# Kernel tuning notes

Measured on AMD Instinct MI355X. Metric: run time of the kernel, lower is better.

The kernel has to match this reference:

```python
import math
import jax, jax.numpy as jnp
import numpy as np

B, S, D = 8, 512, 1024        # batch, seq (dec and enc), model dim
HID, NH = 1024, 16            # attention hidden, heads
C = HID // NH                 # per-head channels (self-attn 'attends' over this dim!)
EPS = 1e-5


def setup_inputs() -> dict:
    key = jax.random.key(0)
    ks = jax.random.split(key, 26)
    w = lambda k, sh: (jax.random.normal(k, sh, jnp.float32) * 0.02)
    inp = {
        "x": jax.random.normal(ks[0], (B, S, D), jnp.float32),
        "h": jax.random.normal(ks[1], (B, S, D), jnp.float32),
        # self-attn (AttentionModule) params, stored [in, out]
        "Wq": w(ks[2], (D, HID)), "bq": jnp.zeros((HID,), jnp.float32),
        "Wk": w(ks[3], (D, HID)), "bk": jnp.zeros((HID,), jnp.float32),
        "Wv": w(ks[4], (D, HID)), "bv": jnp.zeros((HID,), jnp.float32),
        "Wo": w(ks[5], (HID, D)), "bo": jnp.zeros((D,), jnp.float32),
        # cross-attn params
        "Wcq": w(ks[6], (D, HID)), "bcq": jnp.zeros((HID,), jnp.float32),
        "Wck": w(ks[7], (D, HID)), "bck": jnp.zeros((HID,), jnp.float32),
        "Wcv": w(ks[8], (D, HID)), "bcv": jnp.zeros((HID,), jnp.float32),
        "Wco": w(ks[9], (HID, D)), "bco": jnp.zeros((D,), jnp.float32),
        "gamma": jnp.ones((D,), jnp.float32), "beta": jnp.zeros((D,), jnp.float32),
        # FFN (two Linears, NO nonlinearity, per original code)
        "W1": w(ks[10], (D, HID)), "b1": jnp.zeros((HID,), jnp.float32),
        "W2": w(ks[11], (HID, D)), "b2": jnp.zeros((D,), jnp.float32),
    }
    return inp


def _layernorm(x, gamma, beta):
    mu = jnp.mean(x, axis=-1, keepdims=True)
    var = jnp.mean(jnp.square(x - mu), axis=-1, keepdims=True)
    return (x - mu) * jax.lax.rsqrt(var + EPS) * gamma + beta


def _self_attn(x, Wq, bq, Wk, bk, Wv, bv, Wo, bo):
    # FAITHFUL to original: reshape [B,S,NH,C]; einsum '...hq,...hk->...hqk' with
    # batch dims [B,S] -> attention over the C channel dim per token, causal mask over channels.
    Q = (x @ Wq + bq).reshape(B, S, NH, C) / math.sqrt(C)
    K = (x @ Wk + bk).reshape(B, S, NH, C)
    V = (x @ Wv + bv).reshape(B, S, NH, C)
    aff = jnp.einsum('bshq,bshk->bshqk', Q, K)            # [B,S,NH,C,C]
    mask = jnp.triu(jnp.full((C, C), -jnp.inf, jnp.float32), k=1)  # -inf above diag, 0 else
    aff = aff + mask
    w = jax.nn.softmax(aff, axis=-1)
    av = jnp.einsum('bshqk,bshk->bshq', w, V)             # [B,S,NH,C]
    return av.reshape(B, S, HID) @ Wo + bo


def _cross_attn(xd, he, Wcq, bcq, Wck, bck, Wcv, bcv, Wco, bco):
    # standard multi-head cross attention, but scaled by sqrt(d_full) per original
    Q = (xd @ Wcq + bcq).reshape(B, S, NH, C).transpose(0, 2, 1, 3)  # [B,NH,Sq,C]
    K = (he @ Wck + bck).reshape(B, S, NH, C).transpose(0, 2, 1, 3)
    V = (he @ Wcv + bcv).reshape(B, S, NH, C).transpose(0, 2, 1, 3)
    scores = jnp.einsum('bhqd,bhkd->bhqk', Q, K) / math.sqrt(HID)
    p = jax.nn.softmax(scores, axis=-1)
    o = jnp.einsum('bhqk,bhkd->bhqd', p, V)               # [B,NH,Sq,C]
    o = o.transpose(0, 2, 1, 3).reshape(B, S, HID)
    return o @ Wco + bco


def reference(x, h, Wq, bq, Wk, bk, Wv, bv, Wo, bo,
              Wcq, bcq, Wck, bck, Wcv, bcv, Wco, bco,
              gamma, beta, W1, b1, W2, b2):
    out = _self_attn(x, Wq, bq, Wk, bk, Wv, bv, Wo, bo) + x
    out = _layernorm(out, gamma, beta)
    out = _cross_attn(out, h, Wcq, bcq, Wck, bck, Wcv, bcv, Wco, bco) + out
    out = _layernorm(out, gamma, beta)
    out = ((out @ W1 + b1) @ W2 + b2) + out
    out = _layernorm(out, gamma, beta)
    return out
```

## Files before the change

kernel.cpp:

```cpp
#include <hip/hip_runtime.h>

typedef __bf16 bf16_t;
typedef bf16_t bf16x8 __attribute__((ext_vector_type(8)));
typedef bf16_t bf16x4 __attribute__((ext_vector_type(4)));
typedef float f32x4 __attribute__((ext_vector_type(4)));

__device__ __forceinline__ void async_copy16(const void* g, void* l) {
  __builtin_amdgcn_global_load_lds(
      (const __attribute__((address_space(1))) unsigned int*)(unsigned long long)g,
      (__attribute__((address_space(3))) unsigned int*)(unsigned int)(unsigned long long)l,
      16, 0, 0);
}

__device__ __forceinline__ float fast_exp2(float x) {
#if __has_builtin(__builtin_amdgcn_exp2f)
  return __builtin_amdgcn_exp2f(x);
#else
  return exp2f(x);
#endif
}

__device__ __forceinline__ unsigned pack_bf16(float x, float y) {
  bf16_t lo = (bf16_t)x, hi = (bf16_t)y;
  unsigned short ul, uh;
  __builtin_memcpy(&ul, &lo, 2);
  __builtin_memcpy(&uh, &hi, 2);
  return (unsigned)ul | ((unsigned)uh << 16);
}

__global__ __launch_bounds__(256) void cast3_bf16_kernel(
    const float* __restrict__ a, const float* __restrict__ b,
    const float* __restrict__ w1, bf16_t* __restrict__ dst1,
    bf16_t* __restrict__ dstw) {
  int i = (blockIdx.x * 256 + threadIdx.x) * 8;
  const float* s;
  bf16_t* d;
  if (i < 4194304) { s = a + i; d = dst1 + i; }
  else if (i < 8388608) { s = b + i - 4194304; d = dst1 + i; }
  else { s = w1 + i - 8388608; d = dstw + (i - 8388608); }
  float4 u = *(const float4*)s;
  float4 v = *(const float4*)(s + 4);
  bf16x8 o;
  o[0]=(bf16_t)u.x; o[1]=(bf16_t)u.y; o[2]=(bf16_t)u.z; o[3]=(bf16_t)u.w;
  o[4]=(bf16_t)v.x; o[5]=(bf16_t)v.y; o[6]=(bf16_t)v.z; o[7]=(bf16_t)v.w;
  *(bf16x8*)d = o;
}

struct SrcPtrs { const float* p[10]; };
__global__ __launch_bounds__(256) void transpose_cast_all(
    SrcPtrs srcs, bf16_t* __restrict__ dstbase) {
  __shared__ float tile[32][33];
  int z = blockIdx.z;
  const float* src = srcs.p[z];
  bf16_t* dst = dstbase + (size_t)z * 1048576;
  float scale = (z == 0) ? 0.125f : ((z == 4) ? 0.03125f : 1.f);
  int bx = blockIdx.x * 32;
  int by = blockIdx.y * 32;
  int tx = threadIdx.x, ty = threadIdx.y;
#pragma unroll
  for (int i = 0; i < 32; i += 8)
    tile[ty + i][tx] = src[(size_t)(by + ty + i) * 1024 + bx + tx];
  __syncthreads();
#pragma unroll
  for (int i = 0; i < 32; i += 8)
    dst[(size_t)(bx + ty + i) * 1024 + by + tx] = (bf16_t)(tile[tx][ty + i] * scale);
}

__global__ __launch_bounds__(256) void prep_bias_kernel(
    const float* __restrict__ bq, const float* __restrict__ bk,
    const float* __restrict__ bv, const float* __restrict__ bck,
    const float* __restrict__ bcv, const float* __restrict__ bcq,
    const bf16_t* __restrict__ wt9, const float* __restrict__ b1,
    const float* __restrict__ b2, float* __restrict__ cb,
    float* __restrict__ cb2) {
  int bid = blockIdx.x;
  if (bid < 28) {
    int i = bid * 256 + threadIdx.x;
    if (i < 1024) cb[i] = bq[i] * 0.125f;
    else if (i < 2048) cb[i] = bk[i - 1024];
    else if (i < 3072) cb[i] = bv[i - 2048];
    else if (i < 4096) cb[i] = bck[i - 3072];
    else if (i < 5120) cb[i] = bcv[i - 4096];
    else if (i < 6144) cb[i] = bcq[i - 5120] * 0.03125f;
    else cb[i] = 0.f;
  } else {
    int n = (bid - 28) * 256 + threadIdx.x;
    const bf16_t* row = wt9 + (size_t)n * 1024;
    float acc = 0.f;
#pragma unroll 4
    for (int h = 0; h < 1024; h += 8) {
      bf16x8 v = *(const bf16x8*)(row + h);
      float4 ba = *(const float4*)(b1 + h);
      float4 bb = *(const float4*)(b1 + h + 4);
      acc += ba.x*(float)v[0] + ba.y*(float)v[1] + ba.z*(float)v[2] + ba.w*(float)v[3]
           + bb.x*(float)v[4] + bb.y*(float)v[5] + bb.z*(float)v[6] + bb.w*(float)v[7];
    }
    cb2[n] = acc + b2[n];
  }
}

template <int BN, int MI, bool HAS_RES, bool TRANS_OUT>
__device__ __forceinline__ void gemm_core(
    const bf16_t* __restrict__ A, const bf16_t* __restrict__ Bt,
    const float* __restrict__ bias, const bf16_t* __restrict__ res,
    bf16_t* __restrict__ C, int ldC, int bm, int bn,
    bf16_t* As, bf16_t* Bs) {
  constexpr int NI = 4;
  int tid = threadIdx.x;
  int w = tid >> 6, lane = tid & 63;
  int fm = lane & 15, fq = lane >> 4;
  int wm = (BN == 128) ? (w >> 1) * 64 : w * 32;
  int wn = (BN == 128) ? (w & 1) * 64 : 0;
  f32x4 acc[MI][NI] = {};
  for (int kt = 0; kt < 1024; kt += 64) {
#pragma unroll
    for (int i = 0; i < 4; i++) {
      int c = i * 256 + tid;
      int row = c >> 3, skg = (c & 7) ^ (row & 7);
      async_copy16(A + (size_t)(bm + row) * 1024 + kt + skg * 8, &As[c * 8]);
    }
#pragma unroll
    for (int i = 0; i < BN / 32; i++) {
      int c = i * 256 + tid;
      int row = c >> 3, skg = (c & 7) ^ (row & 7);
      async_copy16(Bt + (size_t)(bn + row) * 1024 + kt + skg * 8, &Bs[c * 8]);
    }
    __syncthreads();
#pragma unroll
    for (int ks = 0; ks < 2; ks++) {
      bf16x8 af[MI], bfr[NI];
      int kg = ks * 4 + fq;
#pragma unroll
      for (int mi = 0; mi < MI; mi++) {
        int row = wm + mi * 16 + fm;
        af[mi] = *(const bf16x8*)&As[row * 64 + ((kg ^ (row & 7)) * 8)];
      }
#pragma unroll
      for (int ni = 0; ni < NI; ni++) {
        int row = wn + ni * 16 + fm;
        bfr[ni] = *(const bf16x8*)&Bs[row * 64 + ((kg ^ (row & 7)) * 8)];
      }
#pragma unroll
      for (int mi = 0; mi < MI; mi++)
#pragma unroll
        for (int ni = 0; ni < NI; ni++)
          acc[mi][ni] = __builtin_amdgcn_mfma_f32_16x16x32_bf16(
              af[mi], bfr[ni], acc[mi][ni], 0, 0, 0);
    }
    __syncthreads();
  }
#pragma unroll
  for (int mi = 0; mi < MI; mi++) {
#pragma unroll
    for (int ni = 0; ni < NI; ni++) {
      int col = bn + wn + ni * 16 + fm;
      float bv = bias[col];
      if (TRANS_OUT) {
        int rowb = bm + wm + mi * 16 + fq * 4;
        bf16x4 w4;
#pragma unroll
        for (int r = 0; r < 4; r++) w4[r] = (bf16_t)(acc[mi][ni][r] + bv);
        *(bf16x4*)&C[(size_t)col * ldC + rowb] = w4;
      } else {
#pragma unroll
        for (int r = 0; r < 4; r++) {
          int row = bm + wm + mi * 16 + fq * 4 + r;
          float v = acc[mi][ni][r] + bv;
          if (HAS_RES) v += (float)res[(size_t)row * ldC + col];
          C[(size_t)row * ldC + col] = (bf16_t)v;
        }
      }
    }
  }
}

template <int GX, int GY, int BN>
__device__ __forceinline__ void xcd_map(int lin, int& bm, int& bn) {
  constexpr int HX = GX / 2, QY = GY / 4;
  int xcd = lin & 7, idx = lin >> 3;
  int ly = idx / HX, lx = idx - ly * HX;
  bm = ((xcd >> 1) * QY + ly) * 128;
  bn = ((xcd & 1) * HX + lx) * BN;
}

template <bool HAS_RES, bool TRANS_OUT>
__global__ __launch_bounds__(256) void gemm_bf16(
    const bf16_t* __restrict__ A, const bf16_t* __restrict__ Bt,
    const float* __restrict__ bias, const bf16_t* __restrict__ res,
    bf16_t* __restrict__ C, int ldC) {
  __shared__ bf16_t As[128 * 64];
  __shared__ bf16_t Bs[64 * 64];
  int bm, bn;
  xcd_map<16, 32, 64>(blockIdx.x + 16 * blockIdx.y, bm, bn);
  gemm_core<64, 2, HAS_RES, TRANS_OUT>(A, Bt, bias, res, C, ldC, bm, bn, As, Bs);
}

__global__ __launch_bounds__(256) void gemm_qkv_p(
    const bf16_t* __restrict__ xb, const bf16_t* __restrict__ wt0,
    const bf16_t* __restrict__ wt9, const bf16_t* __restrict__ w1bf,
    const float* __restrict__ cb, bf16_t* __restrict__ qkv,
    bf16_t* __restrict__ pt) {
  __shared__ bf16_t smem[2 * 128 * 64];
  int lin = blockIdx.x + 24 * blockIdx.y;
  if (blockIdx.z == 0) {
    int bm, bn;
    xcd_map<24, 32, 128>(lin, bm, bn);
    gemm_core<128, 4, false, false>(xb, wt0, cb, nullptr, qkv, 3072,
                                    bm, bn, smem, smem + 128 * 64);
  } else {
    if (lin >= 128) return;
    gemm_core<64, 2, false, false>(wt9, w1bf, cb + 6144, nullptr, pt, 1024,
                                   (lin >> 4) * 128, (lin & 15) * 64,
                                   smem, smem + 128 * 64);
  }
}

__global__ __launch_bounds__(256) void gemm_cqkv(
    const bf16_t* __restrict__ t1n, const bf16_t* __restrict__ hb,
    const bf16_t* __restrict__ wt4, const float* __restrict__ cb,
    bf16_t* __restrict__ cq, bf16_t* __restrict__ kbuf,
    bf16_t* __restrict__ vt) {
  __shared__ bf16_t As[128 * 64];
  __shared__ bf16_t Bs[64 * 64];
  int lin = blockIdx.x + 48 * blockIdx.y;
  int xcd = lin & 7, idx = lin >> 3;
  int ly = idx / 24, lx = idx - ly * 24;
  int bm = ((xcd >> 1) * 8 + ly) * 128;
  int gx = (xcd & 1) * 24 + lx;
  int region = gx >> 4;
  int bn = (gx & 15) * 64;
  const bf16_t* Bt = wt4 + (size_t)region * 1048576;
  if (region == 2) {
    gemm_core<64, 2, false, true>(hb, Bt, cb + 4096, nullptr, vt, 4096,
                                  bm, bn, As, Bs);
  } else if (region == 1) {
    gemm_core<64, 2, false, false>(hb, Bt, cb + 3072, nullptr, kbuf, 1024,
                                   bm, bn, As, Bs);
  } else {
    gemm_core<64, 2, false, false>(t1n, Bt, cb + 5120, nullptr, cq, 1024,
                                   bm, bn, As, Bs);
  }
}

__global__ __launch_bounds__(256) void self_attn_kernel(
    const bf16_t* __restrict__ QKV, bf16_t* __restrict__ O) {
  __shared__ float2 kv[4][64];
  int tid = threadIdx.x;
  int wu = tid >> 6, lane = tid & 63;
  int unit = blockIdx.x * 4 + wu;
  int m = unit >> 4, h = unit & 15;
  size_t iq = (size_t)m * 3072 + h * 64 + lane;
  float q = (float)QKV[iq] * 1.44269504089f;
  float kk = (float)QKV[iq + 1024];
  float vv = (float)QKV[iq + 2048];
  kv[wu][lane] = make_float2(kk, vv);
  __syncthreads();
  const float2* kvp = kv[wu];
  float l0 = 0.f, l1 = 0.f, o0 = 0.f, o1 = 0.f;
#pragma unroll
  for (int j = 0; j < 64; j += 2) {
    float2 a = kvp[j];
    float2 b = kvp[j + 1];
    float e0 = fast_exp2(q * a.x);
    float e1 = fast_exp2(q * b.x);
    e0 = (j <= lane) ? e0 : 0.f;
    e1 = (j + 1 <= lane) ? e1 : 0.f;
    l0 += e0; o0 = fmaf(e0, a.y, o0);
    l1 += e1; o1 = fmaf(e1, b.y, o1);
  }
  float l = l0 + l1, o = o0 + o1;
  O[(size_t)m * 1024 + h * 64 + lane] = (bf16_t)(o / l);
}

__global__ __launch_bounds__(256) void cross_attn_mfma(
    const bf16_t* __restrict__ Q, const bf16_t* __restrict__ Kb,
    const bf16_t* __restrict__ Vt, bf16_t* __restrict__ O) {
  __shared__ bf16_t Ks[64 * 64];
  __shared__ bf16_t Vs[64 * 64];
  int tid = threadIdx.x;
  int w = tid >> 6, lane = tid & 63;
  int fm = lane & 15, fq = lane >> 4;
  int bh = blockIdx.x;
  int b = bh >> 4, h = bh & 15;
  int q0 = blockIdx.y * 64 + w * 16;
  const bf16_t* Qp = Q + (size_t)(b * 512 + q0 + fm) * 1024 + h * 64 + fq * 8;
  bf16x8 qf0 = *(const bf16x8*)Qp;
  bf16x8 qf1 = *(const bf16x8*)(Qp + 32);
  f32x4 o[4] = {};
  float mx = -1e30f, l = 0.f;
  for (int k0 = 0; k0 < 512; k0 += 64) {
    __syncthreads();
#pragma unroll
    for (int i = 0; i < 2; i++) {
      int c = i * 256 + tid;
      int row = c >> 3, kg = (c & 7) ^ (row & 7);
      async_copy16(Kb + (size_t)(b * 512 + k0 + row) * 1024 + h * 64 + kg * 8,
                   &Ks[c * 8]);
      async_copy16(Vt + (size_t)(h * 64 + row) * 4096 + b * 512 + k0 + kg * 8,
                   &Vs[c * 8]);
    }
    __syncthreads();
    f32x4 s[4] = {};
#pragma unroll
    for (int mt = 0; mt < 4; mt++) {
      int row = mt * 16 + fm;
#pragma unroll
      for (int f = 0; f < 2; f++) {
        int kg = f * 4 + fq;
        bf16x8 kf = *(const bf16x8*)&Ks[row * 64 + ((kg ^ (row & 7)) * 8)];
        s[mt] = __builtin_amdgcn_mfma_f32_16x16x32_bf16(
            kf, (f ? qf1 : qf0), s[mt], 0, 0, 0);
      }
    }
    float smax = -1e30f;
#pragma unroll
    for (int mt = 0; mt < 4; mt++)
#pragma unroll
      for (int r = 0; r < 4; r++) smax = fmaxf(smax, s[mt][r]);
    smax = fmaxf(smax, __shfl_xor(smax, 16, 64));
    smax = fmaxf(smax, __shfl_xor(smax, 32, 64));
    float nm = fmaxf(mx, smax);
    float corr = __expf(mx - nm);
    float ladd = 0.f;
    unsigned pk0[4], pk1[4];
#pragma unroll
    for (int mt = 0; mt < 4; mt++) {
      float p0 = __expf(s[mt][0] - nm);
      float p1 = __expf(s[mt][1] - nm);
      float p2 = __expf(s[mt][2] - nm);
      float p3 = __expf(s[mt][3] - nm);
      ladd += (p0 + p1) + (p2 + p3);
      pk0[mt] = pack_bf16(p0, p1);
      pk1[mt] = pack_bf16(p2, p3);
    }
    ladd += __shfl_xor(ladd, 16, 64);
    ladd += __shfl_xor(ladd, 32, 64);
    l = l * corr + ladd;
#pragma unroll
    for (int ct = 0; ct < 4; ct++)
#pragma unroll
      for (int r = 0; r < 4; r++) o[ct][r] *= corr;
    union U { unsigned u[4]; bf16x8 v; } pf[2];
    int sl0 = ((fq & 1) * 2) * 16 + fm;
    int sl1 = sl0 + 16;
    bool hi = fq >= 2;
#pragma unroll
    for (int f = 0; f < 2; f++) {
      unsigned a0 = (unsigned)__shfl((int)pk0[f * 2],     sl0, 64);
      unsigned b0 = (unsigned)__shfl((int)pk0[f * 2 + 1], sl0, 64);
      unsigned a1 = (unsigned)__shfl((int)pk1[f * 2],     sl0, 64);
      unsigned b1 = (unsigned)__shfl((int)pk1[f * 2 + 1], sl0, 64);
      unsigned a2 = (unsigned)__shfl((int)pk0[f * 2],     sl1, 64);
      unsigned b2 = (unsigned)__shfl((int)pk0[f * 2 + 1], sl1, 64);
      unsigned a3 = (unsigned)__shfl((int)pk1[f * 2],     sl1, 64);
      unsigned b3 = (unsigned)__shfl((int)pk1[f * 2 + 1], sl1, 64);
      pf[f].u[0] = hi ? b0 : a0;
      pf[f].u[1] = hi ? b1 : a1;
      pf[f].u[2] = hi ? b2 : a2;
      pf[f].u[3] = hi ? b3 : a3;
    }
#pragma unroll
    for (int ct = 0; ct < 4; ct++) {
      int row = ct * 16 + fm;
#pragma unroll
      for (int f = 0; f < 2; f++) {
        int kg = f * 4 + fq;
        bf16x8 vf = *(const bf16x8*)&Vs[row * 64 + ((kg ^ (row & 7)) * 8)];
        o[ct] = __builtin_amdgcn_mfma_f32_16x16x32_bf16(vf, pf[f].v, o[ct], 0, 0, 0);
      }
    }
    mx = nm;
  }
  float inv = 1.f / l;
  bf16_t* Op = O + (size_t)(b * 512 + q0 + fm) * 1024 + h * 64 + fq * 4;
#pragma unroll
  for (int ct = 0; ct < 4; ct++) {
    bf16x4 w4;
    w4[0] = (bf16_t)(o[ct][0] * inv);
    w4[1] = (bf16_t)(o[ct][1] * inv);
    w4[2] = (bf16_t)(o[ct][2] * inv);
    w4[3] = (bf16_t)(o[ct][3] * inv);
    *(bf16x4*)(Op + ct * 16) = w4;
  }
}

template <typename OutT>
__global__ __launch_bounds__(256) void ln_kernel(
    const bf16_t* __restrict__ X, const float* __restrict__ gamma,
    const float* __restrict__ beta, OutT* __restrict__ Y) {
  __shared__ float red[8];
  int row = blockIdx.x;
  int tid = threadIdx.x;
  bf16x4 x4 = *(const bf16x4*)(X + (size_t)row * 1024 + tid * 4);
  float4 v = {(float)x4[0], (float)x4[1], (float)x4[2], (float)x4[3]};
  float s = (v.x + v.y) + (v.z + v.w);
  float ss = fmaf(v.x, v.x, fmaf(v.y, v.y, fmaf(v.z, v.z, v.w * v.w)));
#pragma unroll
  for (int off = 32; off > 0; off >>= 1) {
    s  += __shfl_down(s, off, 64);
    ss += __shfl_down(ss, off, 64);
  }
  if ((tid & 63) == 0) { red[tid >> 6] = s; red[4 + (tid >> 6)] = ss; }
  __syncthreads();
  float S  = (red[0] + red[1]) + (red[2] + red[3]);
  float SS = (red[4] + red[5]) + (red[6] + red[7]);
  float mu = S * (1.f / 1024.f);
  float var = SS * (1.f / 1024.f) - mu * mu;
  float inv = rsqrtf(var + 1e-5f);
  float4 g = *(const float4*)(gamma + tid * 4);
  float4 b = *(const float4*)(beta + tid * 4);
  float r0 = (v.x - mu) * inv * g.x + b.x;
  float r1 = (v.y - mu) * inv * g.y + b.y;
  float r2 = (v.z - mu) * inv * g.z + b.z;
  float r3 = (v.w - mu) * inv * g.w + b.w;
  OutT* yp = Y + (size_t)row * 1024 + tid * 4;
  yp[0] = (OutT)r0; yp[1] = (OutT)r1; yp[2] = (OutT)r2; yp[3] = (OutT)r3;
}

extern "C" void kernel_launch(void* const* d_in, const int* in_sizes, int n_in,
                              void* d_out, int out_size, void* d_ws, size_t ws_size,
                              hipStream_t stream) {
  (void)in_sizes; (void)n_in; (void)out_size; (void)ws_size;
  const float* x  = (const float*)d_in[0];
  const float* hh = (const float*)d_in[1];
  SrcPtrs sp;
  sp.p[0] = (const float*)d_in[2];  sp.p[1] = (const float*)d_in[4];
  sp.p[2] = (const float*)d_in[6];  sp.p[3] = (const float*)d_in[8];
  sp.p[4] = (const float*)d_in[10]; sp.p[5] = (const float*)d_in[12];
  sp.p[6] = (const float*)d_in[14]; sp.p[7] = (const float*)d_in[16];
  sp.p[8] = (const float*)d_in[20]; sp.p[9] = (const float*)d_in[22];
  const float* W1f = (const float*)d_in[20];
  const float* bq  = (const float*)d_in[3];
  const float* bk  = (const float*)d_in[5];
  const float* bv  = (const float*)d_in[7];
  const float* bo  = (const float*)d_in[9];
  const float* bck = (const float*)d_in[13];
  const float* bcv = (const float*)d_in[15];
  const float* bcq = (const float*)d_in[11];
  const float* bco = (const float*)d_in[17];
  const float* gamma = (const float*)d_in[18];
  const float* beta  = (const float*)d_in[19];
  const float* b1  = (const float*)d_in[21];
  const float* b2  = (const float*)d_in[23];
  float* out = (float*)d_out;
  char* ws = (char*)d_ws;
  const size_t MB = 1048576;

  bf16_t* wt[10];
  for (int i = 0; i < 10; i++) wt[i] = (bf16_t*)(ws + (size_t)i * 2 * MB);
  float* cb      = (float*)(ws + 20 * MB);
  float* cb2     = (float*)(ws + 20 * MB + 32768);
  bf16_t* xb     = (bf16_t*)(ws + 21 * MB);
  bf16_t* hb     = (bf16_t*)(ws + 29 * MB);
  bf16_t* qkv    = (bf16_t*)(ws + 37 * MB);
  bf16_t* kbuf   = (bf16_t*)(ws + 37 * MB);
  bf16_t* vtbuf  = (bf16_t*)(ws + 45 * MB);
  bf16_t* cqbuf  = (bf16_t*)(ws + 61 * MB);
  bf16_t* attn   = (bf16_t*)(ws + 69 * MB);
  bf16_t* g4     = (bf16_t*)(ws + 77 * MB);
  bf16_t* ptbuf  = (bf16_t*)(ws + 85 * MB);
  bf16_t* w1bf   = (bf16_t*)(ws + 87 * MB);
  bf16_t* t1n    = xb;
  bf16_t* t2n    = hb;
  bf16_t* f2out  = g4;

  cast3_bf16_kernel<<<4608, 256, 0, stream>>>(x, hh, W1f, xb, w1bf);
  transpose_cast_all<<<dim3(32, 32, 10), dim3(32, 8), 0, stream>>>(sp, (bf16_t*)ws);
  prep_bias_kernel<<<32, 256, 0, stream>>>(bq, bk, bv, bck, bcv, bcq,
                                           wt[9], b1, b2, cb, cb2);

  gemm_qkv_p<<<dim3(24, 32, 2), 256, 0, stream>>>(xb, wt[0], wt[9], w1bf, cb, qkv, ptbuf);
  self_attn_kernel<<<16384, 256, 0, stream>>>(qkv, attn);
  gemm_bf16<true, false><<<dim3(16, 32), 256, 0, stream>>>(attn, wt[3], bo, xb, g4, 1024);
  ln_kernel<bf16_t><<<4096, 256, 0, stream>>>(g4, gamma, beta, t1n);
  gemm_cqkv<<<dim3(48, 32), 256, 0, stream>>>(t1n, hb, wt[4], cb, cqbuf, kbuf, vtbuf);
  cross_attn_mfma<<<dim3(128, 8), 256, 0, stream>>>(cqbuf, kbuf, vtbuf, attn);
  gemm_bf16<true, false><<<dim3(16, 32), 256, 0, stream>>>(attn, wt[7], bco, t1n, g4, 1024);
  ln_kernel<bf16_t><<<4096, 256, 0, stream>>>(g4, gamma, beta, t2n);
  gemm_bf16<true, false><<<dim3(16, 32), 256, 0, stream>>>(t2n, ptbuf, cb2, t2n, f2out, 1024);
  ln_kernel<float><<<4096, 256, 0, stream>>>(f2out, gamma, beta, out);
}
```

Baseline: 391.2 us.

## Double-buffer LDS in output GEMMs and merge prep kernel launches

Adds a double-buffered LDS path to the shared GEMM core so the next K tile's async loads overlap the MFMA work on the current tile, with one barrier per step, and uses it for the three 1024x1024 projection GEMMs. The cast and transpose prep kernels are merged into one launch. The QKV launch is reshaped into a flat grid that no longer spawns blocks that exit immediately. Doubling LDS use may reduce occupancy.

```diff
diff --git a/kernel.cpp b/kernel.cpp
--- a/kernel.cpp
+++ b/kernel.cpp
@@ -28,42 +28,45 @@
   return (unsigned)ul | ((unsigned)uh << 16);
 }
 
-__global__ __launch_bounds__(256) void cast3_bf16_kernel(
+struct SrcPtrs { const float* p[10]; };
+__global__ __launch_bounds__(256) void prep_main(
+    SrcPtrs srcs, bf16_t* __restrict__ dstbase,
     const float* __restrict__ a, const float* __restrict__ b,
     const float* __restrict__ w1, bf16_t* __restrict__ dst1,
     bf16_t* __restrict__ dstw) {
-  int i = (blockIdx.x * 256 + threadIdx.x) * 8;
-  const float* s;
-  bf16_t* d;
-  if (i < 4194304) { s = a + i; d = dst1 + i; }
-  else if (i < 8388608) { s = b + i - 4194304; d = dst1 + i; }
-  else { s = w1 + i - 8388608; d = dstw + (i - 8388608); }
-  float4 u = *(const float4*)s;
-  float4 v = *(const float4*)(s + 4);
-  bf16x8 o;
-  o[0]=(bf16_t)u.x; o[1]=(bf16_t)u.y; o[2]=(bf16_t)u.z; o[3]=(bf16_t)u.w;
-  o[4]=(bf16_t)v.x; o[5]=(bf16_t)v.y; o[6]=(bf16_t)v.z; o[7]=(bf16_t)v.w;
-  *(bf16x8*)d = o;
-}
-
-struct SrcPtrs { const float* p[10]; };
-__global__ __launch_bounds__(256) void transpose_cast_all(
-    SrcPtrs srcs, bf16_t* __restrict__ dstbase) {
   __shared__ float tile[32][33];
-  int z = blockIdx.z;
-  const float* src = srcs.p[z];
-  bf16_t* dst = dstbase + (size_t)z * 1048576;
-  float scale = (z == 0) ? 0.125f : ((z == 4) ? 0.03125f : 1.f);
-  int bx = blockIdx.x * 32;
-  int by = blockIdx.y * 32;
-  int tx = threadIdx.x, ty = threadIdx.y;
-#pragma unroll
-  for (int i = 0; i < 32; i += 8)
-    tile[ty + i][tx] = src[(size_t)(by + ty + i) * 1024 + bx + tx];
-  __syncthreads();
-#pragma unroll
-  for (int i = 0; i < 32; i += 8)
-    dst[(size_t)(bx + ty + i) * 1024 + by + tx] = (bf16_t)(tile[tx][ty + i] * scale);
+  int bid = blockIdx.x;
+  int tid = threadIdx.x;
+  if (bid < 10240) {
+    int z = bid >> 10;
+    int rem = bid & 1023;
+    const float* src = srcs.p[z];
+    bf16_t* dst = dstbase + (size_t)z * 1048576;
+    float scale = (z == 0) ? 0.125f : ((z == 4) ? 0.03125f : 1.f);
+    int bx = (rem & 31) * 32;
+    int by = (rem >> 5) * 32;
+    int tx = tid & 31, ty = tid >> 5;
+#pragma unroll
+    for (int i = 0; i < 32; i += 8)
+      tile[ty + i][tx] = src[(size_t)(by + ty + i) * 1024 + bx + tx];
+    __syncthreads();
+#pragma unroll
+    for (int i = 0; i < 32; i += 8)
+      dst[(size_t)(bx + ty + i) * 1024 + by + tx] = (bf16_t)(tile[tx][ty + i] * scale);
+  } else {
+    int i = ((bid - 10240) * 256 + tid) * 8;
+    const float* s;
+    bf16_t* d;
+    if (i < 4194304) { s = a + i; d = dst1 + i; }
+    else if (i < 8388608) { s = b + i - 4194304; d = dst1 + i; }
+    else { s = w1 + i - 8388608; d = dstw + (i - 8388608); }
+    float4 u = *(const float4*)s;
+    float4 v = *(const float4*)(s + 4);
+    bf16x8 o;
+    o[0]=(bf16_t)u.x; o[1]=(bf16_t)u.y; o[2]=(bf16_t)u.z; o[3]=(bf16_t)u.w;
+    o[4]=(bf16_t)v.x; o[5]=(bf16_t)v.y; o[6]=(bf16_t)v.z; o[7]=(bf16_t)v.w;
+    *(bf16x8*)d = o;
+  }
 }
 
 __global__ __launch_bounds__(256) void prep_bias_kernel(
@@ -99,33 +102,40 @@
   }
 }
 
-template <int BN, int MI, bool HAS_RES, bool TRANS_OUT>
+template <int BN, int MI, bool HAS_RES, bool TRANS_OUT, bool DBUF>
 __device__ __forceinline__ void gemm_core(
     const bf16_t* __restrict__ A, const bf16_t* __restrict__ Bt,
     const float* __restrict__ bias, const bf16_t* __restrict__ res,
     bf16_t* __restrict__ C, int ldC, int bm, int bn,
     bf16_t* As, bf16_t* Bs) {
   constexpr int NI = 4;
+  constexpr int ASZ = 128 * 64, BSZ = BN * 64;
   int tid = threadIdx.x;
   int w = tid >> 6, lane = tid & 63;
   int fm = lane & 15, fq = lane >> 4;
   int wm = (BN == 128) ? (w >> 1) * 64 : w * 32;
   int wn = (BN == 128) ? (w & 1) * 64 : 0;
   f32x4 acc[MI][NI] = {};
-  for (int kt = 0; kt < 1024; kt += 64) {
+
+  auto stage = [&](int kt, int half) {
+    bf16_t* Ad = DBUF ? As + half * ASZ : As;
+    bf16_t* Bd = DBUF ? Bs + half * BSZ : Bs;
 #pragma unroll
     for (int i = 0; i < 4; i++) {
       int c = i * 256 + tid;
       int row = c >> 3, skg = (c & 7) ^ (row & 7);
-      async_copy16(A + (size_t)(bm + row) * 1024 + kt + skg * 8, &As[c * 8]);
+      async_copy16(A + (size_t)(bm + row) * 1024 + kt + skg * 8, &Ad[c * 8]);
     }
 #pragma unroll
     for (int i = 0; i < BN / 32; i++) {
       int c = i * 256 + tid;
       int row = c >> 3, skg = (c & 7) ^ (row & 7);
-      async_copy16(Bt + (size_t)(bn + row) * 1024 + kt + skg * 8, &Bs[c * 8]);
-    }
-    __syncthreads();
+      async_copy16(Bt + (size_t)(bn + row) * 1024 + kt + skg * 8, &Bd[c * 8]);
+    }
+  };
+  auto compute = [&](int half) {
+    const bf16_t* Ac = DBUF ? As + half * ASZ : As;
+    const bf16_t* Bc = DBUF ? Bs + half * BSZ : Bs;
 #pragma unroll
     for (int ks = 0; ks < 2; ks++) {
       bf16x8 af[MI], bfr[NI];
@@ -133,12 +143,12 @@
 #pragma unroll
       for (int mi = 0; mi < MI; mi++) {
         int row = wm + mi * 16 + fm;
-        af[mi] = *(const bf16x8*)&As[row * 64 + ((kg ^ (row & 7)) * 8)];
+        af[mi] = *(const bf16x8*)&Ac[row * 64 + ((kg ^ (row & 7)) * 8)];
       }
 #pragma unroll
       for (int ni = 0; ni < NI; ni++) {
         int row = wn + ni * 16 + fm;
-        bfr[ni] = *(const bf16x8*)&Bs[row * 64 + ((kg ^ (row & 7)) * 8)];
+        bfr[ni] = *(const bf16x8*)&Bc[row * 64 + ((kg ^ (row & 7)) * 8)];
       }
 #pragma unroll
       for (int mi = 0; mi < MI; mi++)
@@ -147,8 +157,26 @@
           acc[mi][ni] = __builtin_amdgcn_mfma_f32_16x16x32_bf16(
               af[mi], bfr[ni], acc[mi][ni], 0, 0, 0);
     }
+  };
+
+  if (DBUF) {
+    stage(0, 0);
     __syncthreads();
-  }
+#pragma unroll
+    for (int t = 0; t < 16; t++) {
+      if (t < 15) stage((t + 1) * 64, (t + 1) & 1);
+      compute(t & 1);
+      __syncthreads();
+    }
+  } else {
+    for (int kt = 0; kt < 1024; kt += 64) {
+      stage(kt, 0);
+      __syncthreads();
+      compute(0);
+      __syncthreads();
+    }
+  }
+
 #pragma unroll
   for (int mi = 0; mi < MI; mi++) {
 #pragma unroll
@@ -188,11 +216,11 @@
     const bf16_t* __restrict__ A, const bf16_t* __restrict__ Bt,
     const float* __restrict__ bias, const bf16_t* __restrict__ res,
     bf16_t* __restrict__ C, int ldC) {
-  __shared__ bf16_t As[128 * 64];
-  __shared__ bf16_t Bs[64 * 64];
+  __shared__ bf16_t As[2 * 128 * 64];
+  __shared__ bf16_t Bs[2 * 64 * 64];
   int bm, bn;
   xcd_map<16, 32, 64>(blockIdx.x + 16 * blockIdx.y, bm, bn);
-  gemm_core<64, 2, HAS_RES, TRANS_OUT>(A, Bt, bias, res, C, ldC, bm, bn, As, Bs);
+  gemm_core<64, 2, HAS_RES, TRANS_OUT, true>(A, Bt, bias, res, C, ldC, bm, bn, As, Bs);
 }
 
 __global__ __launch_bounds__(256) void gemm_qkv_p(
@@ -201,17 +229,16 @@
     const float* __restrict__ cb, bf16_t* __restrict__ qkv,
     bf16_t* __restrict__ pt) {
   __shared__ bf16_t smem[2 * 128 * 64];
-  int lin = blockIdx.x + 24 * blockIdx.y;
-  if (blockIdx.z == 0) {
+  int bid = blockIdx.x;
+  if (bid >= 128) {
     int bm, bn;
-    xcd_map<24, 32, 128>(lin, bm, bn);
-    gemm_core<128, 4, false, false>(xb, wt0, cb, nullptr, qkv, 3072,
-                                    bm, bn, smem, smem + 128 * 64);
+    xcd_map<24, 32, 128>(bid - 128, bm, bn);
+    gemm_core<128, 4, false, false, false>(xb, wt0, cb, nullptr, qkv, 3072,
+                                           bm, bn, smem, smem + 128 * 64);
   } else {
-    if (lin >= 128) return;
-    gemm_core<64, 2, false, false>(wt9, w1bf, cb + 6144, nullptr, pt, 1024,
-                                   (lin >> 4) * 128, (lin & 15) * 64,
-                                   smem, smem + 128 * 64);
+    gemm_core<64, 2, false, false, false>(wt9, w1bf, cb + 6144, nullptr, pt, 1024,
+                                          (bid >> 4) * 128, (bid & 15) * 64,
+                                          smem, smem + 128 * 64);
   }
 }
 
@@ -231,14 +258,14 @@
   int bn = (gx & 15) * 64;
   const bf16_t* Bt = wt4 + (size_t)region * 1048576;
   if (region == 2) {
-    gemm_core<64, 2, false, true>(hb, Bt, cb + 4096, nullptr, vt, 4096,
-                                  bm, bn, As, Bs);
+    gemm_core<64, 2, false, true, false>(hb, Bt, cb + 4096, nullptr, vt, 4096,
+                                         bm, bn, As, Bs);
   } else if (region == 1) {
-    gemm_core<64, 2, false, false>(hb, Bt, cb + 3072, nullptr, kbuf, 1024,
-                                   bm, bn, As, Bs);
+    gemm_core<64, 2, false, false, false>(hb, Bt, cb + 3072, nullptr, kbuf, 1024,
+                                          bm, bn, As, Bs);
   } else {
-    gemm_core<64, 2, false, false>(t1n, Bt, cb + 5120, nullptr, cq, 1024,
-                                   bm, bn, As, Bs);
+    gemm_core<64, 2, false, false, false>(t1n, Bt, cb + 5120, nullptr, cq, 1024,
+                                          bm, bn, As, Bs);
   }
 }
 
@@ -464,12 +491,11 @@
   bf16_t* t2n    = hb;
   bf16_t* f2out  = g4;
 
-  cast3_bf16_kernel<<<4608, 256, 0, stream>>>(x, hh, W1f, xb, w1bf);
-  transpose_cast_all<<<dim3(32, 32, 10), dim3(32, 8), 0, stream>>>(sp, (bf16_t*)ws);
+  prep_main<<<14848, 256, 0, stream>>>(sp, (bf16_t*)ws, x, hh, W1f, xb, w1bf);
   prep_bias_kernel<<<32, 256, 0, stream>>>(bq, bk, bv, bck, bcv, bcq,
                                            wt[9], b1, b2, cb, cb2);
 
-  gemm_qkv_p<<<dim3(24, 32, 2), 256, 0, stream>>>(xb, wt[0], wt[9], w1bf, cb, qkv, ptbuf);
+  gemm_qkv_p<<<896, 256, 0, stream>>>(xb, wt[0], wt[9], w1bf, cb, qkv, ptbuf);
   self_attn_kernel<<<16384, 256, 0, stream>>>(qkv, attn);
   gemm_bf16<true, false><<<dim3(16, 32), 256, 0, stream>>>(attn, wt[3], bo, xb, g4, 1024);
   ln_kernel<bf16_t><<<4096, 256, 0, stream>>>(g4, gamma, beta, t1n);
```

Measured after the change: 364.0 us. 1.07x faster.
